# Optimization experiments

Hardware: AMD Instinct MI355X
Metric: run time of the kernel (lower is better)

Reference implementation:

```python
import jax, jax.numpy as jnp
import numpy as np

TGT, BSZ, E = 2048, 4, 1024
NUM_HEADS = 16
HEAD_DIM = E // NUM_HEADS


def setup_inputs() -> dict:
    key = jax.random.key(0)
    ks = jax.random.split(key, 5)
    return {
        "query": jax.random.normal(ks[0], (TGT, BSZ, E), dtype=jnp.float32),
        "key": jax.random.normal(ks[1], (TGT, BSZ, E), dtype=jnp.float32),
        "value": jax.random.normal(ks[2], (TGT, BSZ, E), dtype=jnp.float32),
        "in_proj_weight": jax.random.normal(ks[3], (3 * E, E), dtype=jnp.float32) * (1.0 / np.sqrt(E)),
        "in_proj_bias": jnp.zeros((3 * E,), dtype=jnp.float32),
        "out_proj_weight": jax.random.normal(ks[4], (E, E), dtype=jnp.float32) * (1.0 / np.sqrt(E)),
        "out_proj_bias": jnp.zeros((E,), dtype=jnp.float32),
    }


def reference(query, key, value, in_proj_weight, in_proj_bias, out_proj_weight, out_proj_bias):
    tgt_len, bsz, embed_dim = query.shape
    src_len = key.shape[0]
    h, hd = NUM_HEADS, embed_dim // NUM_HEADS

    w_q, w_k, w_v = jnp.split(in_proj_weight, 3, axis=0)
    b_q, b_k, b_v = jnp.split(in_proj_bias, 3, axis=0)
    q = query @ w_q.T + b_q   # (Nt, B, E)
    k = key @ w_k.T + b_k     # (Ns, B, E)
    v = value @ w_v.T + b_v

    # (L, B, E) -> (B*H, L, hd)
    q = q.reshape(tgt_len, bsz * h, hd).transpose(1, 0, 2)
    k = k.reshape(src_len, bsz * h, hd).transpose(1, 0, 2)
    v = v.reshape(src_len, bsz * h, hd).transpose(1, 0, 2)

    q = q / jnp.sqrt(jnp.asarray(hd, dtype=q.dtype))
    attn = jnp.einsum('bte,bse->bts', q, k)          # (B*H, Nt, Ns)
    attn = jax.nn.softmax(attn, axis=-1)
    out = jnp.einsum('bts,bse->bte', attn, v)        # (B*H, Nt, hd)

    out = out.transpose(1, 0, 2).reshape(tgt_len, bsz, embed_dim)
    out = out @ out_proj_weight.T + out_proj_bias    # (Nt, B, out_dim)

    avg_weights = attn.reshape(bsz, h, tgt_len, src_len).mean(axis=1)
    return (out, avg_weights)
```

## Files before the change

### kernel.cpp

```cpp
#include <hip/hip_runtime.h>
#include <hip/hip_bf16.h>
#include <hip/hip_fp16.h>

#define TGT 2048
#define BSZ 4
#define EMB 1024
#define NH  16
#define HD  64
#define NTOK (TGT*BSZ)
#define BH   (BSZ*NH)

typedef unsigned short u16;
typedef __attribute__((ext_vector_type(8))) short    s16x8;
typedef __attribute__((ext_vector_type(8))) _Float16 f16x8;
typedef __attribute__((ext_vector_type(2))) _Float16 f16x2;
typedef __attribute__((ext_vector_type(4))) float    f32x4;

#define MFMA_BF16(a,b,c) __builtin_amdgcn_mfma_f32_16x16x32_bf16(a,b,c,0,0,0)
#define MFMA_F16(a,b,c)  __builtin_amdgcn_mfma_f32_16x16x32_f16(a,b,c,0,0,0)

#define GLOAD_LDS16(gsrc, ldst) \
  __builtin_amdgcn_global_load_lds((const __attribute__((address_space(1))) unsigned int*)(gsrc), \
                                   (__attribute__((address_space(3))) unsigned int*)(ldst), 16, 0, 0)

__device__ __forceinline__ void split_one(float x, u16& h, u16& l) {
  __hip_bfloat16 hb = __float2bfloat16(x);
  float hf = __bfloat162float(hb);
  __hip_bfloat16 lb = __float2bfloat16(x - hf);
  h = *reinterpret_cast<u16*>(&hb);
  l = *reinterpret_cast<u16*>(&lb);
}

__global__ __launch_bounds__(256) void split_kernel(const float* __restrict__ x,
    u16* __restrict__ hi, u16* __restrict__ lo, int n4) {
  int i = blockIdx.x * 256 + threadIdx.x;
  if (i >= n4) return;
  float4 v = reinterpret_cast<const float4*>(x)[i];
  ushort4 h, l;
  split_one(v.x, h.x, l.x);
  split_one(v.y, h.y, l.y);
  split_one(v.z, h.z, l.z);
  split_one(v.w, h.w, l.w);
  reinterpret_cast<ushort4*>(hi)[i] = h;
  reinterpret_cast<ushort4*>(lo)[i] = l;
}

template<int EPI>
__global__ __launch_bounds__(256) void gemm_split(
    const u16* __restrict__ Ah, const u16* __restrict__ Al,
    const u16* __restrict__ Bh, const u16* __restrict__ Bl,
    const float* __restrict__ bias, float scale, void* __restrict__ outp, int K)
{
  __shared__ __align__(16) u16 AhS[128][40];
  __shared__ __align__(16) u16 AlS[128][40];
  __shared__ __align__(16) u16 BhS[64][40];
  __shared__ __align__(16) u16 BlS[64][40];
  const int tid  = threadIdx.x;
  const int bm0  = blockIdx.y * 128;
  const int bn0  = blockIdx.x * 64;
  const int wave = tid >> 6, lane = tid & 63, lr = lane & 15, lg = lane >> 4;

  f32x4 zero = {0.f, 0.f, 0.f, 0.f};
  f32x4 acc[2][4];
  #pragma unroll
  for (int i = 0; i < 2; i++)
    #pragma unroll
    for (int j = 0; j < 4; j++) acc[i][j] = zero;

  for (int kt = 0; kt < K; kt += 32) {
    __syncthreads();
    #pragma unroll
    for (int i = 0; i < 2; i++) {
      int c = tid + i*256, r = c >> 2, co = (c & 3) * 8;
      *(uint4*)&AhS[r][co] = *(const uint4*)&Ah[(size_t)(bm0 + r)*K + kt + co];
      *(uint4*)&AlS[r][co] = *(const uint4*)&Al[(size_t)(bm0 + r)*K + kt + co];
    }
    {
      int r = tid >> 2, co = (tid & 3) * 8;
      *(uint4*)&BhS[r][co] = *(const uint4*)&Bh[(size_t)(bn0 + r)*K + kt + co];
      *(uint4*)&BlS[r][co] = *(const uint4*)&Bl[(size_t)(bn0 + r)*K + kt + co];
    }
    __syncthreads();
    s16x8 ah[2], al[2], bh[4], bl[4];
    #pragma unroll
    for (int mf = 0; mf < 2; mf++) {
      ah[mf] = *(const s16x8*)&AhS[wave*32 + mf*16 + lr][lg*8];
      al[mf] = *(const s16x8*)&AlS[wave*32 + mf*16 + lr][lg*8];
    }
    #pragma unroll
    for (int nf = 0; nf < 4; nf++) {
      bh[nf] = *(const s16x8*)&BhS[nf*16 + lr][lg*8];
      bl[nf] = *(const s16x8*)&BlS[nf*16 + lr][lg*8];
    }
    #pragma unroll
    for (int mf = 0; mf < 2; mf++)
      #pragma unroll
      for (int nf = 0; nf < 4; nf++) {
        acc[mf][nf] = MFMA_BF16(al[mf], bh[nf], acc[mf][nf]);
        acc[mf][nf] = MFMA_BF16(ah[mf], bl[nf], acc[mf][nf]);
        acc[mf][nf] = MFMA_BF16(ah[mf], bh[nf], acc[mf][nf]);
      }
  }
  #pragma unroll
  for (int mf = 0; mf < 2; mf++)
    #pragma unroll
    for (int nf = 0; nf < 4; nf++)
      #pragma unroll
      for (int r = 0; r < 4; r++) {
        int m = bm0 + wave*32 + mf*16 + lg*4 + r;
        int n = bn0 + nf*16 + lr;
        float v = (acc[mf][nf][r] + bias[n]) * scale;
        if constexpr (EPI == 0) {
          int t = m >> 2, b = m & 3, h = n >> 6, d = n & 63;
          ((_Float16*)outp)[(size_t)((b*NH + h)*TGT + t)*HD + d] = (_Float16)v;
        } else if constexpr (EPI == 1) {
          int s = m >> 2, b = m & 3, h = n >> 6, d = n & 63;
          ((_Float16*)outp)[(size_t)((b*NH + h)*HD + d)*TGT + s] = (_Float16)v;
        } else {
          ((float*)outp)[(size_t)m*EMB + n] = v;
        }
      }
}

__global__ __launch_bounds__(256) void flash_kernel(
    const _Float16* __restrict__ Qf, const _Float16* __restrict__ Kf,
    const _Float16* __restrict__ Vt, u16* __restrict__ Oh, u16* __restrict__ Ol,
    float* __restrict__ lse)
{
  __shared__ __align__(16) _Float16 Qs[64][72];
  __shared__ __align__(16) _Float16 Ks[64][72];
  __shared__ __align__(16) _Float16 Vs[64][72];
  __shared__ __align__(16) _Float16 Ps[4][16][72];
  const int tid = threadIdx.x, wave = tid >> 6, lane = tid & 63, lr = lane & 15, lg = lane >> 4;
  const int bh = blockIdx.y, t0 = blockIdx.x * 64;
  const int b = bh >> 4, h = bh & 15;

  #pragma unroll
  for (int i = 0; i < 2; i++) {
    int c = tid + i*256, r = c >> 3, co = (c & 7) * 8;
    *(uint4*)&Qs[r][co] = *(const uint4*)&Qf[((size_t)bh*TGT + t0 + r)*HD + co];
  }
  float m_run = -1e30f, l_run = 0.f;
  f32x4 zero = {0.f, 0.f, 0.f, 0.f};
  f32x4 accO[4];
  #pragma unroll
  for (int i = 0; i < 4; i++) accO[i] = zero;

  for (int s0 = 0; s0 < TGT; s0 += 64) {
    __syncthreads();
    #pragma unroll
    for (int i = 0; i < 2; i++) {
      int c = tid + i*256, r = c >> 3, co = (c & 7) * 8;
      *(uint4*)&Ks[r][co] = *(const uint4*)&Kf[((size_t)bh*TGT + s0 + r)*HD + co];
      *(uint4*)&Vs[r][co] = *(const uint4*)&Vt[((size_t)bh*HD + r)*TGT + s0 + co];
    }
    __syncthreads();
    f32x4 sacc[4];
    #pragma unroll
    for (int sf = 0; sf < 4; sf++) sacc[sf] = zero;
    #pragma unroll
    for (int sf = 0; sf < 4; sf++)
      #pragma unroll
      for (int kf = 0; kf < 2; kf++) {
        f16x8 a = *(const f16x8*)&Ks[sf*16 + lr][kf*32 + lg*8];
        f16x8 q = *(const f16x8*)&Qs[wave*16 + lr][kf*32 + lg*8];
        sacc[sf] = MFMA_F16(a, q, sacc[sf]);
      }
    float pm = -1e30f;
    #pragma unroll
    for (int sf = 0; sf < 4; sf++)
      #pragma unroll
      for (int r = 0; r < 4; r++) pm = fmaxf(pm, sacc[sf][r]);
    pm = fmaxf(pm, __shfl_xor(pm, 16, 64));
    pm = fmaxf(pm, __shfl_xor(pm, 32, 64));
    float m_new = fmaxf(m_run, pm);
    float fsc = exp2f(m_run - m_new);
    float psum = 0.f;
    #pragma unroll
    for (int sf = 0; sf < 4; sf++)
      #pragma unroll
      for (int r = 0; r < 4; r++) {
        float p = exp2f(sacc[sf][r] - m_new);
        sacc[sf][r] = p;
        psum += p;
      }
    psum += __shfl_xor(psum, 16, 64);
    psum += __shfl_xor(psum, 32, 64);
    l_run = l_run * fsc + psum;
    m_run = m_new;
    #pragma unroll
    for (int sf = 0; sf < 4; sf++) {
      f16x2 p01 = { (_Float16)sacc[sf][0], (_Float16)sacc[sf][1] };
      f16x2 p23 = { (_Float16)sacc[sf][2], (_Float16)sacc[sf][3] };
      *(f16x2*)&Ps[wave][lr][sf*16 + lg*4]     = p01;
      *(f16x2*)&Ps[wave][lr][sf*16 + lg*4 + 2] = p23;
    }
    float fr[4];
    #pragma unroll
    for (int r = 0; r < 4; r++) fr[r] = __shfl(fsc, lg*4 + r, 64);
    #pragma unroll
    for (int df = 0; df < 4; df++) {
      accO[df][0] *= fr[0]; accO[df][1] *= fr[1];
      accO[df][2] *= fr[2]; accO[df][3] *= fr[3];
    }
    f16x8 pa0 = *(const f16x8*)&Ps[wave][lr][lg*8];
    f16x8 pa1 = *(const f16x8*)&Ps[wave][lr][32 + lg*8];
    #pragma unroll
    for (int df = 0; df < 4; df++) {
      f16x8 v0 = *(const f16x8*)&Vs[df*16 + lr][lg*8];
      f16x8 v1 = *(const f16x8*)&Vs[df*16 + lr][32 + lg*8];
      accO[df] = MFMA_F16(pa0, v0, accO[df]);
      accO[df] = MFMA_F16(pa1, v1, accO[df]);
    }
  }
  float linv = 1.f / l_run;
  float rl[4];
  #pragma unroll
  for (int r = 0; r < 4; r++) rl[r] = __shfl(linv, lg*4 + r, 64);
  #pragma unroll
  for (int df = 0; df < 4; df++)
    #pragma unroll
    for (int r = 0; r < 4; r++) {
      float o = accO[df][r] * rl[r];
      int t = t0 + wave*16 + lg*4 + r;
      int d = df*16 + lr;
      size_t idx = (size_t)(t*BSZ + b)*EMB + h*HD + d;
      u16 hh, ll;
      split_one(o, hh, ll);
      Oh[idx] = hh; Ol[idx] = ll;
    }
  if (lane < 16)
    lse[(size_t)bh*TGT + t0 + wave*16 + lane] = m_run + log2f(l_run);
}

__global__ __launch_bounds__(256) void avg_kernel(
    const _Float16* __restrict__ Qf, const _Float16* __restrict__ Kf,
    const float* __restrict__ lse, float* __restrict__ avgO)
{
  __shared__ __align__(16) _Float16 Qs[128][64];
  __shared__ __align__(16) _Float16 Ks[128][64];
  __shared__ float lses[NH][128];
  const int tid = threadIdx.x, wave = tid >> 6, lane = tid & 63, lr = lane & 15, lg = lane >> 4;

  int fid = blockIdx.x;
  int nid = (fid & 7) * 128 + (fid >> 3);
  int st = nid & 15, tt = (nid >> 4) & 15, b = nid >> 8;
  int s0 = st * 128, t0 = tt * 128;

  #pragma unroll
  for (int i = 0; i < 8; i++) {
    int idx = tid + i * 256;
    int hh = idx >> 7, t = idx & 127;
    lses[hh][t] = lse[(size_t)(b*NH + hh)*TGT + t0 + t];
  }

  f32x4 zero = {0.f, 0.f, 0.f, 0.f};
  f32x4 acc[2][8];
  #pragma unroll
  for (int i = 0; i < 2; i++)
    #pragma unroll
    for (int j = 0; j < 8; j++) acc[i][j] = zero;

  const int rQ = wave * 32;
  const int srcsub = (((lane & 7) ^ (lane >> 3)) << 4) + (lane >> 3) * 128;

  for (int h = 0; h < NH; h++) {
    __syncthreads();
    {
      const char* qb = (const char*)(Qf + ((size_t)(b*NH + h)*TGT + t0) * HD);
      const char* kb = (const char*)(Kf + ((size_t)(b*NH + h)*TGT + s0) * HD);
      const char* gb = (wave < 2) ? qb : kb;
      char* lb = (char*)((wave < 2) ? &Qs[0][0] : &Ks[0][0]);
      const int half = (wave & 1) * 8;
      #pragma unroll
      for (int j = 0; j < 8; j++) {
        int J = half + j;
        GLOAD_LDS16(gb + (size_t)J * 1024 + srcsub, lb + J * 1024);
      }
    }
    __syncthreads();

    float lsr[2][4];
    #pragma unroll
    for (int mf = 0; mf < 2; mf++)
      #pragma unroll
      for (int r = 0; r < 4; r++)
        lsr[mf][r] = lses[h][rQ + mf*16 + lg*4 + r];

    f16x8 aq[2][2];
    #pragma unroll
    for (int mf = 0; mf < 2; mf++)
      #pragma unroll
      for (int kf = 0; kf < 2; kf++) {
        int row = rQ + mf*16 + lr;
        int cb = ((kf*4 + lg) ^ (row & 7)) << 4;
        aq[mf][kf] = *(const f16x8*)((const char*)&Qs[0][0] + row*128 + cb);
      }
    #pragma unroll
    for (int nf = 0; nf < 8; nf++) {
      f32x4 s4[2] = {zero, zero};
      #pragma unroll
      for (int kf = 0; kf < 2; kf++) {
        int row = nf*16 + lr;
        int cb = ((kf*4 + lg) ^ (row & 7)) << 4;
        f16x8 bk = *(const f16x8*)((const char*)&Ks[0][0] + row*128 + cb);
        s4[0] = MFMA_F16(aq[0][kf], bk, s4[0]);
        s4[1] = MFMA_F16(aq[1][kf], bk, s4[1]);
      }
      #pragma unroll
      for (int mf = 0; mf < 2; mf++)
        #pragma unroll
        for (int r = 0; r < 4; r++)
          acc[mf][nf][r] += exp2f(s4[mf][r] - lsr[mf][r]);
    }
  }

  #pragma unroll
  for (int mf = 0; mf < 2; mf++)
    #pragma unroll
    for (int nf = 0; nf < 8; nf++)
      #pragma unroll
      for (int r = 0; r < 4; r++) {
        int t = t0 + rQ + mf*16 + lg*4 + r;
        int s = s0 + nf*16 + lr;
        avgO[((size_t)b*TGT + t)*TGT + s] = acc[mf][nf][r] * (1.f/16.f);
      }
}

extern "C" void kernel_launch(void* const* d_in, const int* in_sizes, int n_in,
                              void* d_out, int out_size, void* d_ws, size_t ws_size,
                              hipStream_t stream) {
  const float* query = (const float*)d_in[0];
  const float* key_  = (const float*)d_in[1];
  const float* value = (const float*)d_in[2];
  const float* ipw   = (const float*)d_in[3];
  const float* ipb   = (const float*)d_in[4];
  const float* opw   = (const float*)d_in[5];
  const float* opb   = (const float*)d_in[6];
  float* out = (float*)d_out;
  float* avg = out + (size_t)TGT*BSZ*EMB;

  char* ws = (char*)d_ws;
  size_t o = 0;
  auto alloc = [&](size_t bytes) { char* p = ws + o; o += bytes; return p; };
  u16* Wh  = (u16*)alloc((size_t)3*EMB*EMB*2);
  u16* Wl  = (u16*)alloc((size_t)3*EMB*EMB*2);
  u16* Woh = (u16*)alloc((size_t)EMB*EMB*2);
  u16* Wol = (u16*)alloc((size_t)EMB*EMB*2);
  u16* Xh  = (u16*)alloc((size_t)NTOK*EMB*2);
  u16* Xl  = (u16*)alloc((size_t)NTOK*EMB*2);
  _Float16* Qf = (_Float16*)alloc((size_t)NTOK*EMB*2);
  _Float16* Kf = (_Float16*)alloc((size_t)NTOK*EMB*2);
  _Float16* Vt = (_Float16*)alloc((size_t)NTOK*EMB*2);
  u16* OhA = (u16*)alloc((size_t)NTOK*EMB*2);
  u16* OlA = (u16*)alloc((size_t)NTOK*EMB*2);
  float* lseA = (float*)alloc((size_t)BH*TGT*4);
  (void)ws_size; (void)in_sizes; (void)n_in; (void)out_size;

  const float QSCALE = 0.18033688011112042f;

  split_kernel<<<3*EMB*EMB/1024, 256, 0, stream>>>(ipw, Wh, Wl, 3*EMB*EMB/4);
  split_kernel<<<EMB*EMB/1024, 256, 0, stream>>>(opw, Woh, Wol, EMB*EMB/4);

  dim3 ggrid(EMB/64, NTOK/128);
  split_kernel<<<NTOK*EMB/1024, 256, 0, stream>>>(query, Xh, Xl, NTOK*EMB/4);
  gemm_split<0><<<ggrid, 256, 0, stream>>>(Xh, Xl, Wh, Wl, ipb, QSCALE, (void*)Qf, EMB);
  split_kernel<<<NTOK*EMB/1024, 256, 0, stream>>>(key_, Xh, Xl, NTOK*EMB/4);
  gemm_split<0><<<ggrid, 256, 0, stream>>>(Xh, Xl, Wh + (size_t)EMB*EMB, Wl + (size_t)EMB*EMB,
                                           ipb + EMB, 1.0f, (void*)Kf, EMB);
  split_kernel<<<NTOK*EMB/1024, 256, 0, stream>>>(value, Xh, Xl, NTOK*EMB/4);
  gemm_split<1><<<ggrid, 256, 0, stream>>>(Xh, Xl, Wh + (size_t)2*EMB*EMB, Wl + (size_t)2*EMB*EMB,
                                           ipb + 2*EMB, 1.0f, (void*)Vt, EMB);

  flash_kernel<<<dim3(TGT/64, BH), 256, 0, stream>>>(Qf, Kf, Vt, OhA, OlA, lseA);
  avg_kernel<<<1024, 256, 0, stream>>>(Qf, Kf, lseA, avg);
  gemm_split<2><<<ggrid, 256, 0, stream>>>(OhA, OlA, Woh, Wol, opb, 1.0f, (void*)out, EMB);
}
```

Measured before the change: 778.1 us.

## Widen split-GEMM tile to 128x128 with direct-to-LDS loads and XOR swizzle

The split-bf16 GEMM tile grows from 128x64 to 128x128, halving the grid and doubling B-fragment reuse per A fragment. Global-to-shared copies now use global_load_lds 16-byte transfers into a single interleaved hi/lo buffer with an XOR swizzle to avoid bank conflicts, instead of register-staged stores into padded arrays. The aim is to cut LDS traffic, VGPR staging and global load instructions per MFMA. In exchange it doubles accumulator registers, which may lower occupancy, and there are fewer blocks (512) to spread across the CUs.

```diff
diff --git a/kernel.cpp b/kernel.cpp
--- a/kernel.cpp
+++ b/kernel.cpp
@@ -51,60 +51,71 @@
     const u16* __restrict__ Bh, const u16* __restrict__ Bl,
     const float* __restrict__ bias, float scale, void* __restrict__ outp, int K)
 {
-  __shared__ __align__(16) u16 AhS[128][40];
-  __shared__ __align__(16) u16 AlS[128][40];
-  __shared__ __align__(16) u16 BhS[64][40];
-  __shared__ __align__(16) u16 BlS[64][40];
+  __shared__ __align__(16) u16 As[128*64];
+  __shared__ __align__(16) u16 Bs[128*64];
   const int tid  = threadIdx.x;
   const int bm0  = blockIdx.y * 128;
-  const int bn0  = blockIdx.x * 64;
+  const int bn0  = blockIdx.x * 128;
   const int wave = tid >> 6, lane = tid & 63, lr = lane & 15, lg = lane >> 4;
 
   f32x4 zero = {0.f, 0.f, 0.f, 0.f};
-  f32x4 acc[2][4];
+  f32x4 acc[2][8];
   #pragma unroll
   for (int i = 0; i < 2; i++)
     #pragma unroll
-    for (int j = 0; j < 4; j++) acc[i][j] = zero;
+    for (int j = 0; j < 8; j++) acc[i][j] = zero;
+
+  const u16* srcA[4];
+  const u16* srcB[4];
+  #pragma unroll
+  for (int j = 0; j < 4; j++) {
+    int gi  = tid + j*256;
+    int row = gi >> 3;
+    int lgc = (gi & 7) ^ (row & 7);
+    const u16* baA = (lgc < 4) ? Ah : Al;
+    const u16* baB = (lgc < 4) ? Bh : Bl;
+    srcA[j] = baA + (size_t)(bm0 + row)*K + (lgc & 3)*8;
+    srcB[j] = baB + (size_t)(bn0 + row)*K + (lgc & 3)*8;
+  }
+  char* AsB = (char*)As;
+  char* BsB = (char*)Bs;
+  const int ldsb = wave*1024;
 
   for (int kt = 0; kt < K; kt += 32) {
     __syncthreads();
     #pragma unroll
-    for (int i = 0; i < 2; i++) {
-      int c = tid + i*256, r = c >> 2, co = (c & 3) * 8;
-      *(uint4*)&AhS[r][co] = *(const uint4*)&Ah[(size_t)(bm0 + r)*K + kt + co];
-      *(uint4*)&AlS[r][co] = *(const uint4*)&Al[(size_t)(bm0 + r)*K + kt + co];
-    }
-    {
-      int r = tid >> 2, co = (tid & 3) * 8;
-      *(uint4*)&BhS[r][co] = *(const uint4*)&Bh[(size_t)(bn0 + r)*K + kt + co];
-      *(uint4*)&BlS[r][co] = *(const uint4*)&Bl[(size_t)(bn0 + r)*K + kt + co];
-    }
-    __syncthreads();
-    s16x8 ah[2], al[2], bh[4], bl[4];
+    for (int j = 0; j < 4; j++) {
+      GLOAD_LDS16(srcA[j] + kt, AsB + ldsb + j*4096);
+      GLOAD_LDS16(srcB[j] + kt, BsB + ldsb + j*4096);
+    }
+    __syncthreads();
+
+    s16x8 ah[2], al2[2];
     #pragma unroll
     for (int mf = 0; mf < 2; mf++) {
-      ah[mf] = *(const s16x8*)&AhS[wave*32 + mf*16 + lr][lg*8];
-      al[mf] = *(const s16x8*)&AlS[wave*32 + mf*16 + lr][lg*8];
-    }
-    #pragma unroll
-    for (int nf = 0; nf < 4; nf++) {
-      bh[nf] = *(const s16x8*)&BhS[nf*16 + lr][lg*8];
-      bl[nf] = *(const s16x8*)&BlS[nf*16 + lr][lg*8];
-    }
-    #pragma unroll
-    for (int mf = 0; mf < 2; mf++)
-      #pragma unroll
-      for (int nf = 0; nf < 4; nf++) {
-        acc[mf][nf] = MFMA_BF16(al[mf], bh[nf], acc[mf][nf]);
-        acc[mf][nf] = MFMA_BF16(ah[mf], bl[nf], acc[mf][nf]);
-        acc[mf][nf] = MFMA_BF16(ah[mf], bh[nf], acc[mf][nf]);
-      }
+      int row = wave*32 + mf*16 + lr;
+      const char* rb = AsB + row*128;
+      ah[mf]  = *(const s16x8*)(rb + (((lg    ) ^ (row & 7)) << 4));
+      al2[mf] = *(const s16x8*)(rb + (((lg | 4) ^ (row & 7)) << 4));
+    }
+    #pragma unroll
+    for (int nf = 0; nf < 8; nf++) {
+      int row = nf*16 + lr;
+      const char* rb = BsB + row*128;
+      s16x8 bh8 = *(const s16x8*)(rb + (((lg    ) ^ (row & 7)) << 4));
+      s16x8 bl8 = *(const s16x8*)(rb + (((lg | 4) ^ (row & 7)) << 4));
+      #pragma unroll
+      for (int mf = 0; mf < 2; mf++) {
+        acc[mf][nf] = MFMA_BF16(al2[mf], bh8, acc[mf][nf]);
+        acc[mf][nf] = MFMA_BF16(ah[mf],  bl8, acc[mf][nf]);
+        acc[mf][nf] = MFMA_BF16(ah[mf],  bh8, acc[mf][nf]);
+      }
+    }
   }
   #pragma unroll
   for (int mf = 0; mf < 2; mf++)
     #pragma unroll
-    for (int nf = 0; nf < 4; nf++)
+    for (int nf = 0; nf < 8; nf++)
       #pragma unroll
       for (int r = 0; r < 4; r++) {
         int m = bm0 + wave*32 + mf*16 + lg*4 + r;
@@ -362,7 +373,7 @@
   split_kernel<<<3*EMB*EMB/1024, 256, 0, stream>>>(ipw, Wh, Wl, 3*EMB*EMB/4);
   split_kernel<<<EMB*EMB/1024, 256, 0, stream>>>(opw, Woh, Wol, EMB*EMB/4);
 
-  dim3 ggrid(EMB/64, NTOK/128);
+  dim3 ggrid(EMB/128, NTOK/128);
   split_kernel<<<NTOK*EMB/1024, 256, 0, stream>>>(query, Xh, Xl, NTOK*EMB/4);
   gemm_split<0><<<ggrid, 256, 0, stream>>>(Xh, Xl, Wh, Wl, ipb, QSCALE, (void*)Qf, EMB);
   split_kernel<<<NTOK*EMB/1024, 256, 0, stream>>>(key_, Xh, Xl, NTOK*EMB/4);
```

Result: faster. 714.0 us (-8.2%).
